# Kernel optimization log

Measured on AMD Instinct MI355X. Metric: run time of the kernel, lower is better.

The kernel has to match this reference:

```python
import jax, jax.numpy as jnp
import numpy as np

N = 50000   # nodes
HID = 32    # hidden_channels
H = 8       # heads == num_edge_features (positional-arg aliasing in source)
E = 800000  # message-passing edges
L = 100000  # supervision (label) edges
NEG_SLOPE = 0.2


def gat_layer(x, src, dst, edge_attr, W, a_src, a_dst, We, a_e, b):
    # x: [N, Fin]; W: [Fin, H*C] -> out [N, H*C] (concat heads), PyG GATConv math
    C = W.shape[1] // H
    h = (x @ W).reshape(-1, H, C)                 # [N, H, C]
    al_src = (h * a_src).sum(-1)                  # [N, H]
    al_dst = (h * a_dst).sum(-1)                  # [N, H]
    he = (edge_attr @ We).reshape(-1, H, C)       # [E, H, C]
    al_e = (he * a_e).sum(-1)                     # [E, H]
    alpha = al_src[src] + al_dst[dst] + al_e      # [E, H]
    alpha = jax.nn.leaky_relu(alpha, NEG_SLOPE)
    # segment softmax over destination-node neighborhoods
    amax = jax.ops.segment_max(alpha, dst, num_segments=N)
    amax = jnp.where(jnp.isfinite(amax), amax, 0.0)
    ex = jnp.exp(alpha - amax[dst])
    denom = jax.ops.segment_sum(ex, dst, num_segments=N)
    w = ex / (denom[dst] + 1e-16)                 # [E, H]
    out = jax.ops.segment_sum(h[src] * w[:, :, None], dst, num_segments=N)
    return out.reshape(-1, H * C) + b             # [N, H*C]


def setup_inputs():
    key = jax.random.key(0)
    ks = jax.random.split(key, 24)
    s = 0.1
    d = {}
    d["node_ids"] = jax.random.randint(ks[0], (N,), 0, N)
    d["edge_index"] = jax.random.randint(ks[1], (2, E), 0, N)
    d["edge_label_index"] = jax.random.randint(ks[2], (2, L), 0, N)
    d["topic"] = jax.random.randint(ks[3], (1,), 0, 10)
    d["edge_attr"] = jax.random.normal(ks[4], (E, H))
    d["edge_label_attr"] = jax.random.normal(ks[5], (L, H))
    d["emb"] = jax.random.normal(ks[6], (N, HID)) * s
    d["W1"] = jax.random.normal(ks[7], (HID, H * HID)) * s
    d["a_src1"] = jax.random.normal(ks[8], (H, HID)) * s
    d["a_dst1"] = jax.random.normal(ks[9], (H, HID)) * s
    d["We1"] = jax.random.normal(ks[10], (H, H * HID)) * s
    d["a_e1"] = jax.random.normal(ks[11], (H, HID)) * s
    d["b1"] = jnp.zeros((H * HID,))
    d["lin1_W"] = jax.random.normal(ks[12], (H * HID, HID)) * s
    d["lin1_b"] = jnp.zeros((HID,))
    d["W2"] = jax.random.normal(ks[13], (HID, H * HID)) * s
    d["a_src2"] = jax.random.normal(ks[14], (H, HID)) * s
    d["a_dst2"] = jax.random.normal(ks[15], (H, HID)) * s
    d["We2"] = jax.random.normal(ks[16], (H, H * HID)) * s
    d["a_e2"] = jax.random.normal(ks[17], (H, HID)) * s
    d["b2"] = jnp.zeros((H * HID,))
    d["lin5_W"] = jax.random.normal(ks[18], (H * HID, H)) * s
    d["lin5_b"] = jnp.zeros((H,))
    d["clf_W"] = jax.random.normal(ks[19], (2 * H, H)) * s
    d["clf_b"] = jnp.zeros((H,))
    return d


def reference(node_ids, edge_index, edge_label_index, topic, edge_attr, edge_label_attr, emb, W1, a_src1, a_dst1, We1, a_e1, b1, lin1_W, lin1_b, W2, a_src2, a_dst2, We2, a_e2, b2, lin5_W, lin5_b, clf_W, clf_b):
    src, dst = edge_index[0], edge_index[1]
    x = emb[node_ids]                                                   # [N, HID]
    x = jax.nn.relu(gat_layer(x, src, dst, edge_attr, W1, a_src1, a_dst1, We1, a_e1, b1))
    x = x @ lin1_W + lin1_b                                             # dropout(p=0.1) is identity in eval
    x = jax.nn.relu(gat_layer(x, src, dst, edge_attr, W2, a_src2, a_dst2, We2, a_e2, b2))
    x = x @ lin5_W + lin5_b                                             # [N, H]
    fu = x[edge_label_index[0]]                                         # [L, H]
    fm = x[edge_label_index[1]]                                         # [L, H]
    fu = jnp.concatenate([fu, edge_label_attr], axis=-1) @ clf_W + clf_b
    return jax.nn.sigmoid((fu * fm).sum(-1))                            # [L]
```

## Files before the change

### kernel.cpp

```cpp
#include <hip/hip_runtime.h>
#include <hip/hip_bf16.h>

#define HC    256
#define FIN   32
#define NH    8
#define GROUP 8
#define CAP   192

typedef __hip_bfloat16 bf16;

__device__ __forceinline__ float blo(unsigned int u) { return __uint_as_float(u << 16); }
__device__ __forceinline__ float bhi(unsigned int u) { return __uint_as_float(u & 0xffff0000u); }

__global__ void count_kernel(const int* __restrict__ dst, int* __restrict__ cnt, int E_) {
  int e = blockIdx.x * blockDim.x + threadIdx.x;
  if (e < E_) atomicAdd(&cnt[dst[e]], 1);
}

__global__ __launch_bounds__(256) void
scan_partial(const int* __restrict__ cnt, int* __restrict__ tmp,
             int* __restrict__ bsum, int N_) {
  __shared__ int part[256];
  int t = threadIdx.x, i = blockIdx.x * 256 + t;
  int v = (i < N_) ? cnt[i] : 0;
  part[t] = v;
  __syncthreads();
#pragma unroll
  for (int off = 1; off < 256; off <<= 1) {
    int u = (t >= off) ? part[t - off] : 0;
    __syncthreads();
    part[t] += u;
    __syncthreads();
  }
  if (i < N_) tmp[i] = part[t];
  if (t == 255) bsum[blockIdx.x] = part[255];
}

__global__ __launch_bounds__(1024) void
scan_bsum(int* __restrict__ bsum, int NB) {
  __shared__ int part[1024];
  int t = threadIdx.x;
  int v = (t < NB) ? bsum[t] : 0;
  part[t] = v;
  __syncthreads();
  for (int off = 1; off < 1024; off <<= 1) {
    int u = (t >= off) ? part[t - off] : 0;
    __syncthreads();
    part[t] += u;
    __syncthreads();
  }
  if (t < NB) bsum[t] = part[t] - v;
}

__global__ __launch_bounds__(256) void
scan_final(const int* __restrict__ cnt, const int* __restrict__ tmp,
           const int* __restrict__ bsum, int* __restrict__ rowptr,
           int* __restrict__ fill, int N_, int E_) {
  int t = threadIdx.x, i = blockIdx.x * 256 + t;
  if (i < N_) {
    int ex = bsum[blockIdx.x] + tmp[i] - cnt[i];
    rowptr[i] = ex;
    fill[i] = ex;
  }
  if (i == 0) rowptr[N_] = E_;
}

__global__ void scatter_kernel(const int* __restrict__ src, const int* __restrict__ dst,
                               int* __restrict__ fill, const float* __restrict__ edge_attr,
                               int* __restrict__ srcs, float* __restrict__ eattr_s, int E_) {
  int e = blockIdx.x * blockDim.x + threadIdx.x;
  if (e < E_) {
    int pos = atomicAdd(&fill[dst[e]], 1);
    srcs[pos] = src[e];
    const float4* ep = (const float4*)(edge_attr + (size_t)e * NH);
    float4 a0 = ep[0], a1 = ep[1];
    float4* op = (float4*)(eattr_s + (size_t)pos * NH);
    op[0] = a0; op[1] = a1;
  }
}

__global__ void fold_kernel(const float* __restrict__ We1, const float* __restrict__ ae1,
                            const float* __restrict__ We2, const float* __restrict__ ae2,
                            const float* __restrict__ W1, const float* __restrict__ as1,
                            const float* __restrict__ ad1,
                            const float* __restrict__ W2, const float* __restrict__ as2,
                            const float* __restrict__ ad2,
                            float* __restrict__ M) {
  for (int idx = threadIdx.x; idx < 1152; idx += 256) {
    const float* A; const float* V; int i;
    if (idx < 64)       { i = idx;       A = We1; V = ae1; }
    else if (idx < 128) { i = idx - 64;  A = We2; V = ae2; }
    else if (idx < 384) { i = idx - 128; A = W1;  V = as1; }
    else if (idx < 640) { i = idx - 384; A = W1;  V = ad1; }
    else if (idx < 896) { i = idx - 640; A = W2;  V = as2; }
    else                { i = idx - 896; A = W2;  V = ad2; }
    int k = i >> 3, h = i & 7;
    float s = 0.f;
    for (int c = 0; c < FIN; ++c)
      s = fmaf(A[k * HC + h * FIN + c], V[h * FIN + c], s);
    M[idx] = s;
  }
}

__global__ __launch_bounds__(256) void
prep1_kernel(const float* __restrict__ emb, const int* __restrict__ node_ids,
             const float* __restrict__ P,
             bf16* __restrict__ xq, float* __restrict__ alsrc,
             float* __restrict__ aldst, int N_) {
  __shared__ float xs[8][33];
  int t = threadIdx.x, n0 = blockIdx.x * 8;
  int nl = t >> 5, c = t & 31;
  int n = n0 + nl;
  if (n < N_) {
    float v = emb[(size_t)node_ids[n] * FIN + c];
    xq[(size_t)n * FIN + c] = __float2bfloat16(v);
    xs[nl][c] = v;
  }
  __syncthreads();
  if (t < 64) {
    int nl2 = t >> 3, h = t & 7;
    int n2 = n0 + nl2;
    if (n2 < N_) {
      float sa = 0.f, sd = 0.f;
#pragma unroll
      for (int k = 0; k < FIN; ++k) {
        float x = xs[nl2][k];
        sa = fmaf(x, P[k * 8 + h], sa);
        sd = fmaf(x, P[256 + k * 8 + h], sd);
      }
      alsrc[(size_t)n2 * NH + h] = sa;
      aldst[(size_t)n2 * NH + h] = sd;
    }
  }
}

template <int K, int LOG2K, bool LOGITS>
__global__ __launch_bounds__(256) void
agg_kernel(const int* __restrict__ rowptr, const int* __restrict__ srcs,
           const float* __restrict__ eattr,
           const float* __restrict__ Mg,
           const float* __restrict__ alsrc, const float* __restrict__ aldst,
           const bf16* __restrict__ xq,
           const float* __restrict__ W, const float* __restrict__ b,
           const float* __restrict__ Wlin, const float* __restrict__ blin,
           float* __restrict__ xoutf, bf16* __restrict__ xqn,
           const float* __restrict__ Pn,
           float* __restrict__ alsrcn, float* __restrict__ aldstn, int N_) {
  __shared__ __align__(16) char smem[25600];
  unsigned int* xsu = (unsigned int*)smem;
  float* wsf   = (float*)(smem + 12288);
  float* Ms    = (float*)(smem + 18432);
  float* ald_s = (float*)(smem + 18688);
  float* zs   = (float*)smem;
  float* gs   = (float*)(smem + 8192);
  float* red  = (float*)(smem + 16384);
  float* xrow = (float*)(smem + 24576);

  int t = threadIdx.x;
  int n0 = blockIdx.x * GROUP;
  int w = t >> 6, l = t & 63, h = l >> 3, q = l & 7;

  int rp[GROUP + 1];
#pragma unroll
  for (int i = 0; i <= GROUP; ++i) {
    int nn = n0 + i;
    rp[i] = rowptr[(nn <= N_) ? nn : N_];
  }
  int nA = n0 + w * 2;
  int e0  = rowptr[(nA     <= N_) ? nA     : N_];
  int e1  = rowptr[(nA + 1 <= N_) ? nA + 1 : N_];
  int e2g = rowptr[(nA + 2 <= N_) ? nA + 2 : N_];

  if (t < 64) Ms[t] = Mg[t];
  if (t < GROUP * NH) {
    int nn = n0 + (t >> 3);
    ald_s[t] = (nn < N_) ? aldst[(size_t)nn * NH + (t & 7)] : 0.f;
  }
  __syncthreads();

  float4 acc0 = make_float4(0.f, 0.f, 0.f, 0.f);
  float4 acc1 = make_float4(0.f, 0.f, 0.f, 0.f);
  float dn0 = 0.f, dn1 = 0.f;

  int beg = rp[0], end = rp[GROUP];
  for (int cbeg = beg; cbeg < end; cbeg += CAP) {
    int clen = end - cbeg; if (clen > CAP) clen = CAP;

    int ntask = clen * 8;
    for (int idx = t; idx < ntask; idx += 256) {
      int e = idx >> 3, c4 = idx & 7;
      int s = srcs[cbeg + e];
      uint2 v = *(const uint2*)(xq + (size_t)s * FIN + c4 * 4);
      *(uint2*)&xsu[e * 16 + c4 * 2] = v;
    }
    for (int eb2 = 0; eb2 < clen; eb2 += 128) {
      int e2 = eb2 + (t >> 1), half = t & 1;
      if (e2 < clen) {
        int j = cbeg + e2;
        int ii = 0;
#pragma unroll
        for (int c = 1; c < GROUP; ++c) ii += (j >= rp[c]) ? 1 : 0;
        int sn = srcs[j];
        float4 eah = *(const float4*)(eattr + (size_t)j * NH + half * 4);
        float4 ash = *(const float4*)(alsrc + (size_t)sn * NH + half * 4);
        float eaf[4] = {eah.x, eah.y, eah.z, eah.w};
        float ea[8];
#pragma unroll
        for (int c = 0; c < 4; ++c) {
          float other = __shfl_xor(eaf[c], 1, 64);
          ea[half * 4 + c] = eaf[c];
          ea[(1 - half) * 4 + c] = other;
        }
        float asf[4] = {ash.x, ash.y, ash.z, ash.w};
        float o[4];
#pragma unroll
        for (int i4 = 0; i4 < 4; ++i4) {
          int hh = half * 4 + i4;
          float al = 0.f;
#pragma unroll
          for (int kk = 0; kk < NH; ++kk) al = fmaf(ea[kk], Ms[kk * NH + hh], al);
          float a = asf[i4] + ald_s[ii * NH + hh] + al;
          a = (a >= 0.f) ? a : 0.2f * a;
          o[i4] = __expf(a);
        }
        *(float4*)&wsf[e2 * 8 + half * 4] = make_float4(o[0], o[1], o[2], o[3]);
      }
    }
    __syncthreads();
    {
      int lo = e0 - cbeg; if (lo < 0) lo = 0;
      int hi = e1 - cbeg; if (hi > clen) hi = clen;
#pragma unroll 4
      for (int le = lo; le < hi; ++le) {
        float wv = wsf[le * 8 + h];
        uint2 u = *(const uint2*)&xsu[le * 16 + q * 2];
        acc0.x = fmaf(blo(u.x), wv, acc0.x);
        acc0.y = fmaf(bhi(u.x), wv, acc0.y);
        acc0.z = fmaf(blo(u.y), wv, acc0.z);
        acc0.w = fmaf(bhi(u.y), wv, acc0.w);
        dn0 += wv;
      }
    }
    {
      int lo = e1 - cbeg; if (lo < 0) lo = 0;
      int hi = e2g - cbeg; if (hi > clen) hi = clen;
#pragma unroll 4
      for (int le = lo; le < hi; ++le) {
        float wv = wsf[le * 8 + h];
        uint2 u = *(const uint2*)&xsu[le * 16 + q * 2];
        acc1.x = fmaf(blo(u.x), wv, acc1.x);
        acc1.y = fmaf(bhi(u.x), wv, acc1.y);
        acc1.z = fmaf(blo(u.y), wv, acc1.z);
        acc1.w = fmaf(bhi(u.y), wv, acc1.w);
        dn1 += wv;
      }
    }
    __syncthreads();
  }

  float rd0 = 1.0f / (dn0 + 1e-16f);
  float rd1 = 1.0f / (dn1 + 1e-16f);
  *(float4*)&zs[(w * 2 + 0) * 256 + l * 4] =
      make_float4(acc0.x * rd0, acc0.y * rd0, acc0.z * rd0, acc0.w * rd0);
  *(float4*)&zs[(w * 2 + 1) * 256 + l * 4] =
      make_float4(acc1.x * rd1, acc1.y * rd1, acc1.z * rd1, acc1.w * rd1);
  __syncthreads();

  int hE = t >> 5;
  float g[GROUP];
#pragma unroll
  for (int i = 0; i < GROUP; ++i) g[i] = b[t];
#pragma unroll
  for (int k4 = 0; k4 < 8; ++k4) {
    float za[GROUP][4];
#pragma unroll
    for (int i = 0; i < GROUP; ++i)
      *(float4*)za[i] = *(const float4*)&zs[i * 256 + hE * 32 + k4 * 4];
#pragma unroll
    for (int kk = 0; kk < 4; ++kk) {
      float wv = W[(k4 * 4 + kk) * HC + t];
#pragma unroll
      for (int i = 0; i < GROUP; ++i) g[i] = fmaf(za[i][kk], wv, g[i]);
    }
  }
#pragma unroll
  for (int i = 0; i < GROUP; ++i) gs[i * 256 + t] = (g[i] > 0.f) ? g[i] : 0.f;
  __syncthreads();

  {
    int kk = t & (K - 1), r = t >> LOG2K;
    float part[GROUP];
#pragma unroll
    for (int i = 0; i < GROUP; ++i) part[i] = 0.f;
#pragma unroll
    for (int j4 = 0; j4 < K / 4; ++j4) {
      float ga[GROUP][4];
#pragma unroll
      for (int i = 0; i < GROUP; ++i)
        *(float4*)ga[i] = *(const float4*)&gs[i * 256 + r * K + j4 * 4];
#pragma unroll
      for (int jj = 0; jj < 4; ++jj) {
        float wl = Wlin[(r * K + j4 * 4 + jj) * K + kk];
#pragma unroll
        for (int i = 0; i < GROUP; ++i) part[i] = fmaf(ga[i][jj], wl, part[i]);
      }
    }
#pragma unroll
    for (int i = 0; i < GROUP; ++i) red[i * 256 + t] = part[i];
  }
  __syncthreads();

  if (LOGITS) {
    if (t < GROUP * 32) {
      int i = t >> 5, kk = t & 31;
      float s = blin[kk];
#pragma unroll
      for (int r2 = 0; r2 < HC / K; ++r2) s += red[i * 256 + r2 * K + kk];
      int nn = n0 + i;
      if (nn < N_) xqn[(size_t)nn * FIN + kk] = __float2bfloat16(s);
      xrow[t] = s;
    }
    __syncthreads();
    if (t < GROUP * NH) {
      int i = t >> 3, hh = t & 7;
      int nn = n0 + i;
      if (nn < N_) {
        float sa = 0.f, sd = 0.f;
#pragma unroll
        for (int k2 = 0; k2 < FIN; ++k2) {
          float x = xrow[i * 32 + k2];
          sa = fmaf(x, Pn[k2 * 8 + hh], sa);
          sd = fmaf(x, Pn[256 + k2 * 8 + hh], sd);
        }
        alsrcn[(size_t)nn * NH + hh] = sa;
        aldstn[(size_t)nn * NH + hh] = sd;
      }
    }
  } else {
    if (t < GROUP * K) {
      int i = t >> LOG2K, kk = t & (K - 1);
      float s = blin[kk];
#pragma unroll
      for (int r2 = 0; r2 < HC / K; ++r2) s += red[i * 256 + r2 * K + kk];
      int nn = n0 + i;
      if (nn < N_) xoutf[(size_t)nn * K + kk] = s;
    }
  }
}

__global__ void clf_kernel(const int* __restrict__ eli, const float* __restrict__ ela,
                           const float* __restrict__ x2, const float* __restrict__ clfW,
                           const float* __restrict__ clfb, float* __restrict__ out, int L_) {
  int i = blockIdx.x * blockDim.x + threadIdx.x;
  if (i >= L_) return;
  int u = eli[i], m = eli[L_ + i];
  const float4* xup = (const float4*)(x2 + (size_t)u * NH);
  const float4* xmp = (const float4*)(x2 + (size_t)m * NH);
  const float4* eap = (const float4*)(ela + (size_t)i * NH);
  float4 xu0 = xup[0], xu1 = xup[1];
  float4 xm0 = xmp[0], xm1 = xmp[1];
  float4 el0 = eap[0], el1 = eap[1];
  float xu[NH] = {xu0.x, xu0.y, xu0.z, xu0.w, xu1.x, xu1.y, xu1.z, xu1.w};
  float xm[NH] = {xm0.x, xm0.y, xm0.z, xm0.w, xm1.x, xm1.y, xm1.z, xm1.w};
  float el[NH] = {el0.x, el0.y, el0.z, el0.w, el1.x, el1.y, el1.z, el1.w};
  float fu[NH];
#pragma unroll
  for (int kk = 0; kk < NH; ++kk) fu[kk] = clfb[kk];
#pragma unroll
  for (int j = 0; j < NH; ++j) {
#pragma unroll
    for (int kk = 0; kk < NH; ++kk) fu[kk] = fmaf(xu[j], clfW[j * NH + kk], fu[kk]);
  }
#pragma unroll
  for (int j = 0; j < NH; ++j) {
#pragma unroll
    for (int kk = 0; kk < NH; ++kk) fu[kk] = fmaf(el[j], clfW[(NH + j) * NH + kk], fu[kk]);
  }
  float dot = 0.f;
#pragma unroll
  for (int kk = 0; kk < NH; ++kk) dot += fu[kk] * xm[kk];
  out[i] = 1.f / (1.f + expf(-dot));
}

extern "C" void kernel_launch(void* const* d_in, const int* in_sizes, int n_in,
                              void* d_out, int out_size, void* d_ws, size_t ws_size,
                              hipStream_t stream) {
  const int* node_ids   = (const int*)d_in[0];
  const int* edge_index = (const int*)d_in[1];
  const int* eli        = (const int*)d_in[2];
  const float* edge_attr = (const float*)d_in[4];
  const float* ela       = (const float*)d_in[5];
  const float* emb       = (const float*)d_in[6];
  const float* W1     = (const float*)d_in[7];
  const float* a_src1 = (const float*)d_in[8];
  const float* a_dst1 = (const float*)d_in[9];
  const float* We1    = (const float*)d_in[10];
  const float* a_e1   = (const float*)d_in[11];
  const float* b1     = (const float*)d_in[12];
  const float* lin1W  = (const float*)d_in[13];
  const float* lin1b  = (const float*)d_in[14];
  const float* W2     = (const float*)d_in[15];
  const float* a_src2 = (const float*)d_in[16];
  const float* a_dst2 = (const float*)d_in[17];
  const float* We2    = (const float*)d_in[18];
  const float* a_e2   = (const float*)d_in[19];
  const float* b2     = (const float*)d_in[20];
  const float* lin5W  = (const float*)d_in[21];
  const float* lin5b  = (const float*)d_in[22];
  const float* clfW   = (const float*)d_in[23];
  const float* clfb   = (const float*)d_in[24];

  const int N_ = in_sizes[0];
  const int E_ = in_sizes[1] / 2;
  const int L_ = in_sizes[2] / 2;
  const int* src  = edge_index;
  const int* dstp = edge_index + E_;

  char* p = (char*)d_ws;
  auto carve = [&](size_t bytes) -> char* {
    char* r = p;
    p += (bytes + 255) & ~(size_t)255;
    return r;
  };
  bf16*  xq1     = (bf16*)carve((size_t)N_ * FIN * 2);
  bf16*  xq2     = (bf16*)carve((size_t)N_ * FIN * 2);
  float* eattr_s = (float*)carve((size_t)E_ * NH * 4);
  float* alsrc1  = (float*)carve((size_t)N_ * NH * 4);
  float* aldst1  = (float*)carve((size_t)N_ * NH * 4);
  float* alsrc2  = (float*)carve((size_t)N_ * NH * 4);
  float* aldst2  = (float*)carve((size_t)N_ * NH * 4);
  float* x2b     = (float*)carve((size_t)N_ * NH * 4);
  float* Mbuf    = (float*)carve(1152 * 4);
  int*   cnt     = (int*)carve((size_t)N_ * 4);
  int*   rowptr  = (int*)carve((size_t)(N_ + 1) * 4);
  int*   fill    = (int*)carve((size_t)N_ * 4);
  int*   stmp    = (int*)carve((size_t)N_ * 4);
  int*   bsum    = (int*)carve(1024 * 4);
  int*   srcs    = (int*)carve((size_t)E_ * 4);

  hipMemsetAsync(cnt, 0, (size_t)N_ * 4, stream);
  int eb = (E_ + 255) / 256;
  int nb = (N_ + 255) / 256;
  fold_kernel<<<1, 256, 0, stream>>>(We1, a_e1, We2, a_e2, W1, a_src1, a_dst1,
                                     W2, a_src2, a_dst2, Mbuf);
  count_kernel<<<eb, 256, 0, stream>>>(dstp, cnt, E_);
  scan_partial<<<nb, 256, 0, stream>>>(cnt, stmp, bsum, N_);
  scan_bsum<<<1, 1024, 0, stream>>>(bsum, nb);
  scan_final<<<nb, 256, 0, stream>>>(cnt, stmp, bsum, rowptr, fill, N_, E_);
  scatter_kernel<<<eb, 256, 0, stream>>>(src, dstp, fill, edge_attr, srcs, eattr_s, E_);
  prep1_kernel<<<(N_ + 7) / 8, 256, 0, stream>>>(emb, node_ids, Mbuf + 128,
                                                 xq1, alsrc1, aldst1, N_);

  int gb = (N_ + GROUP - 1) / GROUP;
  agg_kernel<32, 5, true><<<gb, 256, 0, stream>>>(
      rowptr, srcs, eattr_s, Mbuf, alsrc1, aldst1, xq1,
      W1, b1, lin1W, lin1b, nullptr, xq2, Mbuf + 640, alsrc2, aldst2, N_);

  agg_kernel<8, 3, false><<<gb, 256, 0, stream>>>(
      rowptr, srcs, eattr_s, Mbuf + 64, alsrc2, aldst2, xq2,
      W2, b2, lin5W, lin5b, x2b, nullptr, nullptr, nullptr, nullptr, N_);

  clf_kernel<<<(L_ + 255) / 256, 256, 0, stream>>>(eli, ela, x2b, clfW, clfb,
                                                   (float*)d_out, L_);
}
```

Baseline: 387.3 us.

## Precompute edge attention logits in scatter and use per-wave edge chunks

The scatter kernel now applies the folded edge-attention matrices for both layers and stores per-edge, per-head logits. The aggregation kernels therefore skip the 8x8 matvec per edge. The aggregation loop is restructured so each wave handles its own two nodes' edges in private 32-edge LDS chunks, replacing block-wide __syncthreads with lgkmcnt waits, and shared memory shrinks with launch bounds requesting higher occupancy. This costs an extra E×8 float buffer written in scatter, and it relies on wave-level ordering of LDS accesses for correctness.

```diff
diff --git a/kernel.cpp b/kernel.cpp
--- a/kernel.cpp
+++ b/kernel.cpp
@@ -5,7 +5,7 @@
 #define FIN   32
 #define NH    8
 #define GROUP 8
-#define CAP   192
+#define CAPW  32
 
 typedef __hip_bfloat16 bf16;
 
@@ -67,15 +67,37 @@
 
 __global__ void scatter_kernel(const int* __restrict__ src, const int* __restrict__ dst,
                                int* __restrict__ fill, const float* __restrict__ edge_attr,
-                               int* __restrict__ srcs, float* __restrict__ eattr_s, int E_) {
+                               const float* __restrict__ M,
+                               int* __restrict__ srcs, float* __restrict__ ale1,
+                               float* __restrict__ ale2, int E_) {
+  __shared__ float Msh[128];
+  if (threadIdx.x < 128) Msh[threadIdx.x] = M[threadIdx.x];
+  __syncthreads();
   int e = blockIdx.x * blockDim.x + threadIdx.x;
   if (e < E_) {
     int pos = atomicAdd(&fill[dst[e]], 1);
     srcs[pos] = src[e];
     const float4* ep = (const float4*)(edge_attr + (size_t)e * NH);
     float4 a0 = ep[0], a1 = ep[1];
-    float4* op = (float4*)(eattr_s + (size_t)pos * NH);
-    op[0] = a0; op[1] = a1;
+    float ea[8] = {a0.x, a0.y, a0.z, a0.w, a1.x, a1.y, a1.z, a1.w};
+    float o1[8], o2[8];
+#pragma unroll
+    for (int h = 0; h < 8; ++h) { o1[h] = 0.f; o2[h] = 0.f; }
+#pragma unroll
+    for (int k = 0; k < 8; ++k) {
+      float x = ea[k];
+#pragma unroll
+      for (int h = 0; h < 8; ++h) {
+        o1[h] = fmaf(x, Msh[k * 8 + h], o1[h]);
+        o2[h] = fmaf(x, Msh[64 + k * 8 + h], o2[h]);
+      }
+    }
+    float4* p1 = (float4*)(ale1 + (size_t)pos * NH);
+    p1[0] = make_float4(o1[0], o1[1], o1[2], o1[3]);
+    p1[1] = make_float4(o1[4], o1[5], o1[6], o1[7]);
+    float4* p2 = (float4*)(ale2 + (size_t)pos * NH);
+    p2[0] = make_float4(o2[0], o2[1], o2[2], o2[3]);
+    p2[1] = make_float4(o2[4], o2[5], o2[6], o2[7]);
   }
 }
 
@@ -135,10 +157,9 @@
 }
 
 template <int K, int LOG2K, bool LOGITS>
-__global__ __launch_bounds__(256) void
+__global__ __launch_bounds__(256, 8) void
 agg_kernel(const int* __restrict__ rowptr, const int* __restrict__ srcs,
-           const float* __restrict__ eattr,
-           const float* __restrict__ Mg,
+           const float* __restrict__ ale,
            const float* __restrict__ alsrc, const float* __restrict__ aldst,
            const bf16* __restrict__ xq,
            const float* __restrict__ W, const float* __restrict__ b,
@@ -146,32 +167,27 @@
            float* __restrict__ xoutf, bf16* __restrict__ xqn,
            const float* __restrict__ Pn,
            float* __restrict__ alsrcn, float* __restrict__ aldstn, int N_) {
-  __shared__ __align__(16) char smem[25600];
+  __shared__ __align__(16) char smem[17408];
   unsigned int* xsu = (unsigned int*)smem;
-  float* wsf   = (float*)(smem + 12288);
-  float* Ms    = (float*)(smem + 18432);
-  float* ald_s = (float*)(smem + 18688);
+  float* wsf   = (float*)(smem + 8192);
+  float* ald_s = (float*)(smem + 12288);
   float* zs   = (float*)smem;
   float* gs   = (float*)(smem + 8192);
-  float* red  = (float*)(smem + 16384);
-  float* xrow = (float*)(smem + 24576);
+  float* red  = (float*)smem;
+  float* xrow = (float*)(smem + 16384);
 
   int t = threadIdx.x;
   int n0 = blockIdx.x * GROUP;
   int w = t >> 6, l = t & 63, h = l >> 3, q = l & 7;
 
-  int rp[GROUP + 1];
-#pragma unroll
-  for (int i = 0; i <= GROUP; ++i) {
-    int nn = n0 + i;
-    rp[i] = rowptr[(nn <= N_) ? nn : N_];
-  }
+  unsigned int* xw  = xsu + w * 512;
+  float*        wsw = wsf + w * 256;
+
   int nA = n0 + w * 2;
   int e0  = rowptr[(nA     <= N_) ? nA     : N_];
   int e1  = rowptr[(nA + 1 <= N_) ? nA + 1 : N_];
   int e2g = rowptr[(nA + 2 <= N_) ? nA + 2 : N_];
 
-  if (t < 64) Ms[t] = Mg[t];
   if (t < GROUP * NH) {
     int nn = n0 + (t >> 3);
     ald_s[t] = (nn < N_) ? aldst[(size_t)nn * NH + (t & 7)] : 0.f;
@@ -182,80 +198,58 @@
   float4 acc1 = make_float4(0.f, 0.f, 0.f, 0.f);
   float dn0 = 0.f, dn1 = 0.f;
 
-  int beg = rp[0], end = rp[GROUP];
-  for (int cbeg = beg; cbeg < end; cbeg += CAP) {
-    int clen = end - cbeg; if (clen > CAP) clen = CAP;
+  for (int cbeg = e0; cbeg < e2g; cbeg += CAPW) {
+    int clen = e2g - cbeg; if (clen > CAPW) clen = CAPW;
 
     int ntask = clen * 8;
-    for (int idx = t; idx < ntask; idx += 256) {
+    for (int idx = l; idx < ntask; idx += 64) {
       int e = idx >> 3, c4 = idx & 7;
       int s = srcs[cbeg + e];
       uint2 v = *(const uint2*)(xq + (size_t)s * FIN + c4 * 4);
-      *(uint2*)&xsu[e * 16 + c4 * 2] = v;
-    }
-    for (int eb2 = 0; eb2 < clen; eb2 += 128) {
-      int e2 = eb2 + (t >> 1), half = t & 1;
+      *(uint2*)&xw[e * 16 + c4 * 2] = v;
+    }
+    {
+      int e2 = l >> 1, half = l & 1;
       if (e2 < clen) {
         int j = cbeg + e2;
-        int ii = 0;
-#pragma unroll
-        for (int c = 1; c < GROUP; ++c) ii += (j >= rp[c]) ? 1 : 0;
+        int ii = (j >= e1) ? 1 : 0;
         int sn = srcs[j];
-        float4 eah = *(const float4*)(eattr + (size_t)j * NH + half * 4);
-        float4 ash = *(const float4*)(alsrc + (size_t)sn * NH + half * 4);
-        float eaf[4] = {eah.x, eah.y, eah.z, eah.w};
-        float ea[8];
-#pragma unroll
-        for (int c = 0; c < 4; ++c) {
-          float other = __shfl_xor(eaf[c], 1, 64);
-          ea[half * 4 + c] = eaf[c];
-          ea[(1 - half) * 4 + c] = other;
-        }
-        float asf[4] = {ash.x, ash.y, ash.z, ash.w};
+        float4 av  = *(const float4*)(ale + (size_t)j * NH + half * 4);
+        float4 as4 = *(const float4*)(alsrc + (size_t)sn * NH + half * 4);
+        float4 ad4 = *(const float4*)&ald_s[(w * 2 + ii) * 8 + half * 4];
         float o[4];
-#pragma unroll
-        for (int i4 = 0; i4 < 4; ++i4) {
-          int hh = half * 4 + i4;
-          float al = 0.f;
-#pragma unroll
-          for (int kk = 0; kk < NH; ++kk) al = fmaf(ea[kk], Ms[kk * NH + hh], al);
-          float a = asf[i4] + ald_s[ii * NH + hh] + al;
-          a = (a >= 0.f) ? a : 0.2f * a;
-          o[i4] = __expf(a);
-        }
-        *(float4*)&wsf[e2 * 8 + half * 4] = make_float4(o[0], o[1], o[2], o[3]);
+        float a0f = av.x + as4.x + ad4.x; a0f = (a0f >= 0.f) ? a0f : 0.2f * a0f;
+        float a1f = av.y + as4.y + ad4.y; a1f = (a1f >= 0.f) ? a1f : 0.2f * a1f;
+        float a2f = av.z + as4.z + ad4.z; a2f = (a2f >= 0.f) ? a2f : 0.2f * a2f;
+        float a3f = av.w + as4.w + ad4.w; a3f = (a3f >= 0.f) ? a3f : 0.2f * a3f;
+        o[0] = __expf(a0f); o[1] = __expf(a1f); o[2] = __expf(a2f); o[3] = __expf(a3f);
+        *(float4*)&wsw[e2 * 8 + half * 4] = make_float4(o[0], o[1], o[2], o[3]);
       }
     }
-    __syncthreads();
-    {
-      int lo = e0 - cbeg; if (lo < 0) lo = 0;
-      int hi = e1 - cbeg; if (hi > clen) hi = clen;
+    asm volatile("s_waitcnt lgkmcnt(0)" ::: "memory");
+
+    int hA = e1 - cbeg; if (hA < 0) hA = 0; if (hA > clen) hA = clen;
 #pragma unroll 4
-      for (int le = lo; le < hi; ++le) {
-        float wv = wsf[le * 8 + h];
-        uint2 u = *(const uint2*)&xsu[le * 16 + q * 2];
-        acc0.x = fmaf(blo(u.x), wv, acc0.x);
-        acc0.y = fmaf(bhi(u.x), wv, acc0.y);
-        acc0.z = fmaf(blo(u.y), wv, acc0.z);
-        acc0.w = fmaf(bhi(u.y), wv, acc0.w);
-        dn0 += wv;
-      }
-    }
-    {
-      int lo = e1 - cbeg; if (lo < 0) lo = 0;
-      int hi = e2g - cbeg; if (hi > clen) hi = clen;
+    for (int le = 0; le < hA; ++le) {
+      float wv = wsw[le * 8 + h];
+      uint2 u = *(const uint2*)&xw[le * 16 + q * 2];
+      acc0.x = fmaf(blo(u.x), wv, acc0.x);
+      acc0.y = fmaf(bhi(u.x), wv, acc0.y);
+      acc0.z = fmaf(blo(u.y), wv, acc0.z);
+      acc0.w = fmaf(bhi(u.y), wv, acc0.w);
+      dn0 += wv;
+    }
 #pragma unroll 4
-      for (int le = lo; le < hi; ++le) {
-        float wv = wsf[le * 8 + h];
-        uint2 u = *(const uint2*)&xsu[le * 16 + q * 2];
-        acc1.x = fmaf(blo(u.x), wv, acc1.x);
-        acc1.y = fmaf(bhi(u.x), wv, acc1.y);
-        acc1.z = fmaf(blo(u.y), wv, acc1.z);
-        acc1.w = fmaf(bhi(u.y), wv, acc1.w);
-        dn1 += wv;
-      }
-    }
-    __syncthreads();
+    for (int le = hA; le < clen; ++le) {
+      float wv = wsw[le * 8 + h];
+      uint2 u = *(const uint2*)&xw[le * 16 + q * 2];
+      acc1.x = fmaf(blo(u.x), wv, acc1.x);
+      acc1.y = fmaf(bhi(u.x), wv, acc1.y);
+      acc1.z = fmaf(blo(u.y), wv, acc1.z);
+      acc1.w = fmaf(bhi(u.y), wv, acc1.w);
+      dn1 += wv;
+    }
+    asm volatile("s_waitcnt lgkmcnt(0)" ::: "memory");
   }
 
   float rd0 = 1.0f / (dn0 + 1e-16f);
@@ -283,6 +277,7 @@
       for (int i = 0; i < GROUP; ++i) g[i] = fmaf(za[i][kk], wv, g[i]);
     }
   }
+  __syncthreads();
 #pragma unroll
   for (int i = 0; i < GROUP; ++i) gs[i * 256 + t] = (g[i] > 0.f) ? g[i] : 0.f;
   __syncthreads();
@@ -424,7 +419,8 @@
   };
   bf16*  xq1     = (bf16*)carve((size_t)N_ * FIN * 2);
   bf16*  xq2     = (bf16*)carve((size_t)N_ * FIN * 2);
-  float* eattr_s = (float*)carve((size_t)E_ * NH * 4);
+  float* ale1_s  = (float*)carve((size_t)E_ * NH * 4);
+  float* ale2_s  = (float*)carve((size_t)E_ * NH * 4);
   float* alsrc1  = (float*)carve((size_t)N_ * NH * 4);
   float* aldst1  = (float*)carve((size_t)N_ * NH * 4);
   float* alsrc2  = (float*)carve((size_t)N_ * NH * 4);
@@ -447,17 +443,18 @@
   scan_partial<<<nb, 256, 0, stream>>>(cnt, stmp, bsum, N_);
   scan_bsum<<<1, 1024, 0, stream>>>(bsum, nb);
   scan_final<<<nb, 256, 0, stream>>>(cnt, stmp, bsum, rowptr, fill, N_, E_);
-  scatter_kernel<<<eb, 256, 0, stream>>>(src, dstp, fill, edge_attr, srcs, eattr_s, E_);
+  scatter_kernel<<<eb, 256, 0, stream>>>(src, dstp, fill, edge_attr, Mbuf,
+                                         srcs, ale1_s, ale2_s, E_);
   prep1_kernel<<<(N_ + 7) / 8, 256, 0, stream>>>(emb, node_ids, Mbuf + 128,
                                                  xq1, alsrc1, aldst1, N_);
 
   int gb = (N_ + GROUP - 1) / GROUP;
   agg_kernel<32, 5, true><<<gb, 256, 0, stream>>>(
-      rowptr, srcs, eattr_s, Mbuf, alsrc1, aldst1, xq1,
+      rowptr, srcs, ale1_s, alsrc1, aldst1, xq1,
       W1, b1, lin1W, lin1b, nullptr, xq2, Mbuf + 640, alsrc2, aldst2, N_);
 
   agg_kernel<8, 3, false><<<gb, 256, 0, stream>>>(
-      rowptr, srcs, eattr_s, Mbuf + 64, alsrc2, aldst2, xq2,
+      rowptr, srcs, ale2_s, alsrc2, aldst2, xq2,
       W2, b2, lin5W, lin5b, x2b, nullptr, nullptr, nullptr, nullptr, N_);
 
   clf_kernel<<<(L_ + 255) / 256, 256, 0, stream>>>(eli, ela, x2b, clfW, clfb,
```

Result: faster. 365.5 us (-5.6%).
